# Kernel optimization log

Hardware: AMD Instinct MI355X
Metric: run time of the kernel (lower is better)

## Reference

```python
import jax, jax.numpy as jnp
import numpy as np

B, RES, C = 4, 128, 256
HW = RES * RES
H_FFT, W_FFT = RES, RES // 2 + 1
NUM_BANDS, GATE_HIDDEN = 6, 128
LN_EPS = 1e-5
FFT_NORM = 'ortho'
INIT_RANGE = 0.02


def _band_info(h_fft, w_fft, nb):
    # static radial band partition of the rFFT2 plane (matches RadialBandGate.__init__)
    yy = np.arange(h_fft, dtype=np.float32)[:, None] / max(h_fft - 1, 1)
    xx = np.arange(w_fft, dtype=np.float32)[None, :] / max(w_fft - 1, 1)
    r = np.sqrt(yy ** 2 + xx ** 2)
    r = r / (r.max() + 1e-8)
    bid = np.minimum(np.floor(r * nb), nb - 1).astype(np.int32).reshape(-1)  # (F,)
    onehot = np.zeros((bid.size, nb), dtype=np.float32)
    onehot[np.arange(bid.size), bid] = 1.0
    counts = np.maximum(onehot.sum(0), 1.0)
    return jnp.asarray(bid), jnp.asarray(onehot), jnp.asarray(counts)

BAND_ID, BAND_ONEHOT, BAND_COUNTS = _band_info(H_FFT, W_FFT, NUM_BANDS)


def setup_inputs() -> dict:
    key = jax.random.key(0)
    ks = jax.random.split(key, 16)
    return {
        'x': jax.random.normal(ks[0], (B, HW, C), jnp.float32),
        'time': jax.random.uniform(ks[1], (B,), jnp.float32),
        'w_real': jax.random.normal(ks[2], (C, C), jnp.float32) * INIT_RANGE,
        'w_imag': jax.random.normal(ks[3], (C, C), jnp.float32) * INIT_RANGE,
        'conv_w': jax.random.normal(ks[4], (C, 1, 3, 3), jnp.float32) * 0.1,  # depthwise
        'lin_w': jax.random.normal(ks[5], (C, C), jnp.float32) * 0.02,
        'lin_b': jnp.zeros((C,), jnp.float32),
        'mlp_w1': jax.random.normal(ks[6], (GATE_HIDDEN, NUM_BANDS), jnp.float32) * 0.3,
        'mlp_b1': jnp.zeros((GATE_HIDDEN,), jnp.float32),
        'mlp_w2': jax.random.normal(ks[7], (NUM_BANDS, GATE_HIDDEN), jnp.float32) * 0.1,
        'mlp_b2': jnp.zeros((NUM_BANDS,), jnp.float32),
        'norm_ww': jax.random.normal(ks[8], (C, 1), jnp.float32) * 0.02,  # ConditionalLayerNorm.weight Linear(1,dim)
        'norm_wb': jnp.ones((C,), jnp.float32),
        'norm_bw': jax.random.normal(ks[9], (C, 1), jnp.float32) * 0.02,
        'norm_bb': jnp.zeros((C,), jnp.float32),
        'kx': jnp.asarray(0.25, jnp.float32),
        'ky': jnp.asarray(0.25, jnp.float32),
    }


def _band_gate(feat, mlp_w1, mlp_b1, mlp_w2, mlp_b2):
    # feat: (B, C, F) real. scatter-add per band via one-hot matmul, mean, MLP, gather back.
    sums = jnp.einsum('bcf,fn->bcn', feat, BAND_ONEHOT)           # (B,C,NB)
    means = sums / (BAND_COUNTS + 1e-6)
    h = jax.nn.relu(jnp.einsum('bcn,hn->bch', means, mlp_w1) + mlp_b1)
    alpha_band = jax.nn.sigmoid(jnp.einsum('bch,nh->bcn', h, mlp_w2) + mlp_b2)
    return alpha_band[:, :, BAND_ID]                               # (B,C,F)


def reference(x, time, w_real, w_imag, conv_w, lin_w, lin_b,
              mlp_w1, mlp_b1, mlp_w2, mlp_b2,
              norm_ww, norm_wb, norm_bw, norm_bb, kx, ky):
    h = w = RES
    x2 = jnp.transpose(x.reshape(B, h, w, C), (0, 3, 1, 2))        # (B,C,h,w)
    Xf = jnp.fft.rfft2(x2, norm=FFT_NORM)                          # (B,C,h_fft,w_fft) complex

    # low-frequency rectangular mask (int(sigmoid(k)*dim) == floor for positive values)
    kx_i = jnp.floor(jax.nn.sigmoid(kx) * H_FFT)
    ky_i = jnp.floor(jax.nn.sigmoid(ky) * W_FFT)
    mask = ((jnp.arange(H_FFT)[:, None] < kx_i) & (jnp.arange(W_FFT)[None, :] < ky_i))
    Xf_low = Xf * mask[None, None].astype(Xf.real.dtype)

    F = H_FFT * W_FFT
    Xf_low_flat = Xf_low.reshape(B, C, F)
    W = w_real + 1j * w_imag                                       # (C,C) complex
    Xf_low_mapped = jnp.einsum('cd,bdf->bcf', W, Xf_low_flat).reshape(B, C, H_FFT, W_FFT)

    Xf_high = Xf - Xf_low
    feat_pred = jnp.abs(jnp.abs(Xf_high).reshape(B, C, F) - jnp.abs(Xf_low).reshape(B, C, F))
    alpha = _band_gate(feat_pred, mlp_w1, mlp_b1, mlp_w2, mlp_b2).reshape(B, C, H_FFT, W_FFT)

    Xf_fused = alpha * Xf_low_mapped + (1.0 - alpha) * Xf_high
    x_spec = jnp.fft.irfft2(Xf_fused, s=(h, w), norm=FFT_NORM)     # (B,C,h,w) real

    # depthwise 3x3 conv, padding=1, no bias
    xl = jax.lax.conv_general_dilated(x2, conv_w, window_strides=(1, 1), padding='SAME',
                                      feature_group_count=C,
                                      dimension_numbers=('NCHW', 'OIHW', 'NCHW'))
    # pointwise linear over channel dim
    xc = jnp.transpose((x @ lin_w.T + lin_b).reshape(B, h, w, C), (0, 3, 1, 2))

    y = jnp.transpose(x_spec + xl + xc, (0, 2, 3, 1)).reshape(B, HW, C)

    # ConditionalLayerNorm
    mean = y.mean(axis=-1, keepdims=True)
    var = (y ** 2).mean(axis=-1, keepdims=True) - mean ** 2
    yn = (y - mean) / jnp.sqrt(var + LN_EPS)
    t = time.reshape(-1, 1)                                        # (B,1)
    weight = (t @ norm_ww.T + norm_wb)[:, None, :]                 # (B,1,C)
    bias = (t @ norm_bw.T + norm_bb)[:, None, :]
    return weight * yn + bias
```

## Files before the change

kernel.cpp:

```cpp
#include <hip/hip_runtime.h>
#include <math.h>

#define B_ 4
#define C_ 256
#define RES_ 128
#define HW_ 16384
#define WF_ 65
#define F_ 8320
#define FP_ 2880

typedef __attribute__((ext_vector_type(8))) short bf16x8;
typedef __attribute__((ext_vector_type(16))) float f32x16;

__device__ __forceinline__ int brev7(int j){ return (int)(__brev((unsigned)j) >> 25); }
__device__ __forceinline__ int brev6(int j){ return (int)(__brev((unsigned)j) >> 26); }

__device__ __forceinline__ short f2bf(float f){
  unsigned u = __float_as_uint(f);
  unsigned r = (u + 0x7FFFu + ((u>>16)&1u)) >> 16;
  return (short)r;
}

__device__ __forceinline__ bf16x8 lds_frag(const short* p){
  union { bf16x8 v; int2 d[2]; } u;
  u.d[0] = *(const int2*)p;
  u.d[1] = *(const int2*)(p+4);
  return u.v;
}
__device__ __forceinline__ void lds_store8(short* p, bf16x8 v){
  union { bf16x8 v; int2 d[2]; } u; u.v = v;
  *(int2*)p = u.d[0]; *(int2*)(p+4) = u.d[1];
}

__device__ __forceinline__ int band_of(int row, int col){
  float yy = __fdiv_rn((float)row, 127.0f);
  float xx = __fdiv_rn((float)col, 64.0f);
  float rr = __fsqrt_rn(__fadd_rn(__fmul_rn(yy,yy), __fmul_rn(xx,xx)));
  float rm = __fadd_rn(__fsqrt_rn(2.0f), 1e-8f);
  float rn = __fdiv_rn(rr, rm);
  int b = (int)floorf(__fmul_rn(rn, 6.0f));
  return b > 5 ? 5 : b;
}

__device__ __forceinline__ float sigmoidf_(float v){ return 1.0f/(1.0f+expf(-v)); }

template<int SGN, int NROWS>
__device__ __forceinline__ void fft128_lds(float2* buf, int rstride, int tid, const float2* tw){
  const int total = NROWS*64;
  #pragma unroll
  for (int stage=0; stage<7; stage++){
    int half = 64 >> stage;
    __syncthreads();
    for (int idx = tid; idx < total; idx += 256){
      int row = idx % NROWS;
      int t   = idx / NROWS;
      int j   = t & (half-1);
      int i0  = ((t >> (6-stage)) << (7-stage)) + j;
      int i1  = i0 + half;
      float2* rb = buf + row*rstride;
      float2 a = rb[i0], b = rb[i1];
      float2 w = tw[j << stage];
      float dx = a.x - b.x, dy = a.y - b.y;
      rb[i0] = make_float2(a.x+b.x, a.y+b.y);
      float ws = (SGN < 0) ? -w.y : w.y;
      rb[i1] = make_float2(dx*w.x - dy*ws, dx*ws + dy*w.x);
    }
  }
  __syncthreads();
}

template<int SGN>
__device__ __forceinline__ float2 wave_fft64(float2 v, const float2* stw, int lane){
  #pragma unroll
  for (int s=0; s<6; s++){
    int H = 32 >> s;
    float ox = __shfl_xor(v.x, H);
    float oy = __shfl_xor(v.y, H);
    bool hi = (lane & H) != 0;
    float2 w = stw[s];
    float ws = (SGN < 0) ? -w.y : w.y;
    float sx = v.x + ox, sy = v.y + oy;
    float dx = ox - v.x, dy = oy - v.y;
    float rx = dx*w.x - dy*ws;
    float ry = dx*ws + dy*w.x;
    v.x = hi ? rx : sx;
    v.y = hi ? ry : sy;
  }
  return v;
}

__device__ __forceinline__ void make_stage_tw(float2* stw, int lane){
  #pragma unroll
  for (int s=0; s<6; s++){
    int H = 32 >> s;
    int t = (lane & (H-1)) << s;
    float sn, cs;
    sincosf(6.283185307179586f*(float)t/64.0f, &sn, &cs);
    stw[s] = make_float2(cs, sn);
  }
}

__global__ __launch_bounds__(1024) void k_transpose(const float* __restrict__ x, float* __restrict__ x2){
  __shared__ float tile[64][65];
  int b = blockIdx.z;
  int hw0 = blockIdx.x*64, c0 = blockIdx.y*64;
  int tx = threadIdx.x, ty = threadIdx.y;
  #pragma unroll
  for (int i=0;i<4;i++){
    int hw = hw0 + ty + i*16;
    tile[ty+i*16][tx] = x[((size_t)b*HW_ + hw)*C_ + c0 + tx];
  }
  __syncthreads();
  #pragma unroll
  for (int i=0;i<4;i++){
    int c = c0 + ty + i*16;
    x2[((size_t)b*C_ + c)*HW_ + hw0 + tx] = tile[tx][ty+i*16];
  }
}

__global__ __launch_bounds__(256) void k_counts(float* __restrict__ counts, unsigned char* __restrict__ bid){
  int tid = threadIdx.x;
  float acc[6] = {0,0,0,0,0,0};
  for (int f = tid; f < F_; f += 256){
    int row = f / WF_, col = f - row*WF_;
    int bnd = band_of(row, col);
    bid[f] = (unsigned char)bnd;
    #pragma unroll
    for (int n=0;n<6;n++) acc[n] += (bnd==n) ? 1.0f : 0.0f;
  }
  __shared__ float red[6][256];
  #pragma unroll
  for (int n=0;n<6;n++) red[n][tid] = acc[n];
  __syncthreads();
  for (int s=128; s>0; s>>=1){
    if (tid < s){
      #pragma unroll
      for (int n=0;n<6;n++) red[n][tid] += red[n][tid+s];
    }
    __syncthreads();
  }
  if (tid < 6) counts[tid] = fmaxf(red[tid][0], 1.0f);
}

__global__ __launch_bounds__(256) void k_wbf16(const float* __restrict__ wre, const float* __restrict__ wim,
                                               const float* __restrict__ lw,
                                               short* __restrict__ Wre, short* __restrict__ Wim,
                                               short* __restrict__ WL){
  int c = blockIdx.x, tid = threadIdx.x, plane = blockIdx.y;
  int idx = c*C_ + tid;
  if (plane == 0)      Wre[idx] = f2bf(wre[idx]);
  else if (plane == 1) Wim[idx] = f2bf(wim[idx]);
  else                 WL[idx]  = f2bf(lw[idx]);
}

__global__ __launch_bounds__(256) void k_fwd_rows(const float* __restrict__ x2, float2* __restrict__ X1){
  int tid = threadIdx.x;
  int lane = tid & 63, wv = tid >> 6;
  float2 stw[6];
  make_stage_tw(stw, lane);
  float sn128, cs128;
  sincosf(6.283185307179586f*(float)lane/128.0f, &sn128, &cs128);
  int slice = blockIdx.x >> 2;
  int r0 = (blockIdx.x & 3) * 32;
  const float* img = x2 + (size_t)slice*HW_ + (size_t)r0*128;
  float2* dst = X1 + (size_t)slice*F_ + (size_t)r0*WF_;
  #pragma unroll
  for (int i=0; i<8; i++){
    int row = wv*8 + i;
    float2 y = *(const float2*)(img + row*128 + lane*2);
    float2 v = wave_fft64<-1>(y, stw, lane);
    int rbk = brev6(lane);
    float2 Yk; Yk.x = __shfl(v.x, rbk); Yk.y = __shfl(v.y, rbk);
    int rbm = brev6((64 - lane) & 63);
    float2 Ym; Ym.x = __shfl(v.x, rbm); Ym.y = __shfl(v.y, rbm);
    float sx = Yk.x + Ym.x, sy = Yk.y - Ym.y;
    float dx = Yk.x - Ym.x, dy = Yk.y + Ym.y;
    dst[row*WF_ + lane] = make_float2(0.5f*(sx - sn128*dx + cs128*dy),
                                      0.5f*(sy - cs128*dx - sn128*dy));
    if (lane == 0)
      dst[row*WF_ + 64] = make_float2(Yk.x - Yk.y, 0.0f);
  }
}

__global__ __launch_bounds__(256) void k_fwd_cols_gate(const float2* __restrict__ X1, float2* __restrict__ Xf,
                                                       const float* __restrict__ counts, const unsigned char* __restrict__ bid,
                                                       const float* __restrict__ w1, const float* __restrict__ b1,
                                                       const float* __restrict__ w2, const float* __restrict__ b2,
                                                       float* __restrict__ alpha){
  __shared__ float2 cbuf[13*129];
  __shared__ float2 tw[64];
  __shared__ float red[6][256];
  __shared__ float means[6], h[128];
  int tid = threadIdx.x;
  if (tid < 64){ float s,c; sincosf(6.283185307179586f*(float)tid/128.0f,&s,&c); tw[tid]=make_float2(c,s); }
  int slice = blockIdx.x;
  const float2* xin = X1 + (size_t)slice*F_;
  float2* xout = Xf + (size_t)slice*F_;
  float acc[6] = {0,0,0,0,0,0};
  for (int chunk=0; chunk<5; chunk++){
    int c0 = chunk*13;
    __syncthreads();
    for (int p = tid; p < 13*128; p += 256){
      int y = p / 13, col = p - y*13;
      cbuf[col*129 + y] = xin[y*WF_ + c0 + col];
    }
    fft128_lds<-1,13>(cbuf, 129, tid, tw);
    for (int p = tid; p < 13*128; p += 256){
      int ky = p / 13, col = p - ky*13, kx = c0 + col;
      float2 v = cbuf[col*129 + brev7(ky)];
      v.x *= 0.0078125f; v.y *= 0.0078125f;
      int f = ky*WF_ + kx;
      xout[f] = v;
      float m = __fsqrt_rn(v.x*v.x + v.y*v.y);
      int bb = (int)bid[f];
      #pragma unroll
      for (int n=0;n<6;n++) acc[n] += (bb==n) ? m : 0.0f;
    }
  }
  __syncthreads();
  #pragma unroll
  for (int n=0;n<6;n++) red[n][tid] = acc[n];
  __syncthreads();
  for (int s=128; s>0; s>>=1){
    if (tid < s){
      #pragma unroll
      for (int n=0;n<6;n++) red[n][tid] += red[n][tid+s];
    }
    __syncthreads();
  }
  if (tid < 6) means[tid] = red[tid][0] / (counts[tid] + 1e-6f);
  __syncthreads();
  if (tid < 128){
    float hv = b1[tid];
    #pragma unroll
    for (int n=0;n<6;n++) hv += means[n]*w1[tid*6+n];
    h[tid] = fmaxf(hv, 0.0f);
  }
  __syncthreads();
  if (tid < 6){
    float o = b2[tid];
    for (int j=0;j<128;j++) o += h[j]*w2[tid*128+j];
    alpha[slice*6 + tid] = sigmoidf_(o);
  }
}

__global__ __launch_bounds__(256) void k_xt(const float2* __restrict__ Xf,
                                            short* __restrict__ XtRe, short* __restrict__ XtIm){
  __shared__ float2 tile[40][129];
  int tid = threadIdx.x;
  int ky = blockIdx.x, d0 = blockIdx.y*128, b = blockIdx.z;
  const float2* xb = Xf + ((size_t)(b*C_ + d0))*F_ + ky*WF_;
  #pragma unroll
  for (int i=0;i<20;i++){
    int p = tid + i*256;
    int d = p / 40, kx = p - d*40;
    tile[kx][d] = xb[(size_t)d*F_ + kx];
  }
  __syncthreads();
  #pragma unroll
  for (int i=0;i<20;i++){
    int p = tid + i*256;
    int kx = p >> 7, d = p & 127;
    float2 v = tile[kx][d];
    size_t o = ((size_t)b*FP_ + ky*40 + kx)*C_ + d0 + d;
    XtRe[o] = f2bf(v.x);
    XtIm[o] = f2bf(v.y);
  }
}

__global__ __launch_bounds__(256) void k_mix_mfma(const short* __restrict__ Wre, const short* __restrict__ Wim,
                                                  const short* __restrict__ XtRe, const short* __restrict__ XtIm,
                                                  const float* __restrict__ kxp, const float* __restrict__ kyp,
                                                  float2* __restrict__ mappedP){
  __shared__ short Are[64][36], Aim[64][36], Bre[64][36], Bim[64][36];
  int tid = threadIdx.x;
  int fp0 = blockIdx.x*64, c0 = blockIdx.y*64, b = blockIdx.z;
  int lane = tid & 63, w = tid >> 6;
  int mt = (w >> 1)*32, nt = (w & 1)*32;
  f32x16 accre = {0.f,0.f,0.f,0.f,0.f,0.f,0.f,0.f,0.f,0.f,0.f,0.f,0.f,0.f,0.f,0.f};
  f32x16 accim = {0.f,0.f,0.f,0.f,0.f,0.f,0.f,0.f,0.f,0.f,0.f,0.f,0.f,0.f,0.f,0.f};
  const short* xrb = XtRe + ((size_t)b*FP_ + fp0)*C_;
  const short* xib = XtIm + ((size_t)b*FP_ + fp0)*C_;
  int row4 = tid >> 2, part = tid & 3;
  for (int kc=0; kc<8; kc++){
    int d0 = kc*32;
    __syncthreads();
    lds_store8(&Are[row4][part*8], *(const bf16x8*)&Wre[(c0+row4)*C_ + d0 + part*8]);
    lds_store8(&Aim[row4][part*8], *(const bf16x8*)&Wim[(c0+row4)*C_ + d0 + part*8]);
    lds_store8(&Bre[row4][part*8], *(const bf16x8*)&xrb[(size_t)row4*C_ + d0 + part*8]);
    lds_store8(&Bim[row4][part*8], *(const bf16x8*)&xib[(size_t)row4*C_ + d0 + part*8]);
    __syncthreads();
    #pragma unroll
    for (int ks=0; ks<2; ks++){
      int koff = ks*16 + (lane>>5)*8;
      bf16x8 are = lds_frag(&Are[mt + (lane&31)][koff]);
      bf16x8 aim = lds_frag(&Aim[mt + (lane&31)][koff]);
      bf16x8 bre = lds_frag(&Bre[nt + (lane&31)][koff]);
      bf16x8 bim = lds_frag(&Bim[nt + (lane&31)][koff]);
      bf16x8 naim;
      { union { bf16x8 v; unsigned u[4]; } t1, t2; t1.v = aim;
        #pragma unroll
        for (int j=0;j<4;j++) t2.u[j] = t1.u[j] ^ 0x80008000u;
        naim = t2.v; }
      accre = __builtin_amdgcn_mfma_f32_32x32x16_bf16(are,  bre, accre, 0,0,0);
      accre = __builtin_amdgcn_mfma_f32_32x32x16_bf16(naim, bim, accre, 0,0,0);
      accim = __builtin_amdgcn_mfma_f32_32x32x16_bf16(are,  bim, accim, 0,0,0);
      accim = __builtin_amdgcn_mfma_f32_32x32x16_bf16(aim,  bre, accim, 0,0,0);
    }
  }
  float rowlim = floorf(sigmoidf_(kxp[0])*128.0f);
  float collim = floorf(sigmoidf_(kyp[0])*65.0f);
  int n = fp0 + nt + (lane & 31);
  int ky = n / 40, kx = n - ky*40;
  bool live = ((float)ky < rowlim) && ((float)kx < collim);
  #pragma unroll
  for (int reg=0; reg<16; reg++){
    int r = (reg & 3) + 8*(reg >> 2) + 4*(lane >> 5);
    int c = c0 + mt + r;
    if (live)
      mappedP[((size_t)(b*C_ + c))*FP_ + n] = make_float2(accre[reg], accim[reg]);
  }
}

__global__ __launch_bounds__(256) void k_pw_mfma(const float* __restrict__ x, const short* __restrict__ WL,
                                                  const float* __restrict__ lb, float* __restrict__ xcs){
  __shared__ short As[64][36], Bs[64][36];
  int tid = threadIdx.x;
  int hw0 = blockIdx.x*64, c0 = blockIdx.y*64, b = blockIdx.z;
  int lane = tid & 63, w = tid >> 6;
  int mt = (w >> 1)*32, nt = (w & 1)*32;
  f32x16 acc = {0.f,0.f,0.f,0.f,0.f,0.f,0.f,0.f,0.f,0.f,0.f,0.f,0.f,0.f,0.f,0.f};
  const float* xb = x + ((size_t)b*HW_ + hw0)*C_;
  int row4 = tid >> 2, part = tid & 3;
  for (int kc=0; kc<8; kc++){
    int d0 = kc*32;
    __syncthreads();
    lds_store8(&As[row4][part*8], *(const bf16x8*)&WL[(c0+row4)*C_ + d0 + part*8]);
    {
      const float* src = &xb[(size_t)row4*C_ + d0 + part*8];
      float4 va = *(const float4*)src;
      float4 vb = *(const float4*)(src+4);
      bf16x8 bv;
      bv[0]=f2bf(va.x); bv[1]=f2bf(va.y); bv[2]=f2bf(va.z); bv[3]=f2bf(va.w);
      bv[4]=f2bf(vb.x); bv[5]=f2bf(vb.y); bv[6]=f2bf(vb.z); bv[7]=f2bf(vb.w);
      lds_store8(&Bs[row4][part*8], bv);
    }
    __syncthreads();
    #pragma unroll
    for (int ks=0; ks<2; ks++){
      int koff = ks*16 + (lane>>5)*8;
      bf16x8 a  = lds_frag(&As[mt + (lane&31)][koff]);
      bf16x8 bb = lds_frag(&Bs[nt + (lane&31)][koff]);
      acc = __builtin_amdgcn_mfma_f32_32x32x16_bf16(a, bb, acc, 0,0,0);
    }
  }
  int n = hw0 + nt + (lane & 31);
  #pragma unroll
  for (int reg=0; reg<16; reg++){
    int r = (reg & 3) + 8*(reg >> 2) + 4*(lane >> 5);
    int c = c0 + mt + r;
    xcs[((size_t)(b*C_ + c))*HW_ + n] = acc[reg] + lb[c];
  }
}

__global__ __launch_bounds__(256) void k_inv_cols(float2* __restrict__ XfY, const float2* __restrict__ mappedP,
                                                  const float* __restrict__ alpha, const unsigned char* __restrict__ bid,
                                                  const float* __restrict__ kxp, const float* __restrict__ kyp){
  __shared__ float2 cbuf[13*129];
  __shared__ float2 tw[64];
  __shared__ float al[6];
  int tid = threadIdx.x;
  int chunk = blockIdx.x, slice = blockIdx.y;
  int c0 = chunk*13;
  if (tid < 64){ float s,c; sincosf(6.283185307179586f*(float)tid/128.0f,&s,&c); tw[tid]=make_float2(c,s); }
  if (tid < 6) al[tid] = alpha[slice*6 + tid];
  float rowlim = floorf(sigmoidf_(kxp[0])*128.0f);
  float collim = floorf(sigmoidf_(kyp[0])*65.0f);
  __syncthreads();
  float2* xfb = XfY + (size_t)slice*F_;
  const float2* mpb = mappedP + (size_t)slice*FP_;
  for (int p = tid; p < 13*128; p += 256){
    int ky = p / 13, col = p - ky*13, kx = c0 + col;
    int f = ky*WF_ + kx;
    float a = al[(int)bid[f]];
    bool inm = ((float)ky < rowlim) && ((float)kx < collim);
    float2 v;
    if (inm){ v = mpb[ky*40 + kx]; v.x *= a; v.y *= a; }
    else    { v = xfb[f]; float om = 1.0f - a; v.x *= om; v.y *= om; }
    cbuf[col*129 + ky] = v;
  }
  fft128_lds<1,13>(cbuf, 129, tid, tw);
  for (int p = tid; p < 13*128; p += 256){
    int y = p / 13, col = p - y*13;
    xfb[y*WF_ + c0 + col] = cbuf[col*129 + brev7(y)];
  }
}

__global__ __launch_bounds__(256) void k_inv_rows(const float2* __restrict__ Y1, const float* __restrict__ xcs,
                                                  const float* __restrict__ x2, const float* __restrict__ cw,
                                                  float* __restrict__ sbuf){
  __shared__ float ct[34*128];
  int tid = threadIdx.x;
  int lane = tid & 63, wv = tid >> 6;
  float2 stw[6];
  make_stage_tw(stw, lane);
  float sn128, cs128;
  sincosf(6.283185307179586f*(float)lane/128.0f, &sn128, &cs128);
  int slice = blockIdx.x >> 2;
  int ch = slice & 255;
  int r0 = (blockIdx.x & 3) * 32;
  const float* img = x2 + (size_t)slice*HW_;
  #pragma unroll
  for (int q=0;q<17;q++){
    int p = tid + q*256;
    int row = p >> 7, xx = p & 127;
    int sr = r0 - 1 + row;
    ct[p] = ((unsigned)sr < 128u) ? img[sr*128+xx] : 0.0f;
  }
  float w9[9];
  #pragma unroll
  for (int k=0;k<9;k++) w9[k] = cw[ch*9+k];
  __syncthreads();
  const float2* src = Y1 + (size_t)slice*F_ + (size_t)r0*WF_;
  size_t gbase = (size_t)slice*HW_ + (size_t)r0*128;
  #pragma unroll
  for (int i=0;i<8;i++){
    int row = wv*8 + i;
    const float2* rs = src + row*WF_;
    float2 a = rs[lane];
    float2 b = rs[64 - lane];
    if (lane == 0){ a.y = 0.0f; b.y = 0.0f; }
    float sx = a.x + b.x, sy = a.y - b.y;
    float dx = a.x - b.x, dy = a.y + b.y;
    float2 yk = make_float2(0.5f*(sx - sn128*dx - cs128*dy),
                            0.5f*(sy + cs128*dx - sn128*dy));
    float2 v = wave_fft64<1>(yk, stw, lane);
    int rbk = brev6(lane);
    float2 z; z.x = __shfl(v.x, rbk); z.y = __shfl(v.y, rbk);
    int xx = lane << 1;
    float c0 = 0.0f, c1 = 0.0f;
    #pragma unroll
    for (int dy2=0; dy2<3; dy2++){
      const float* cr = &ct[(row+dy2)*128];
      float l  = (xx>0)    ? cr[xx-1] : 0.0f;
      float mm = cr[xx];
      float r  = cr[xx+1];
      float rr = (xx<126)  ? cr[xx+2] : 0.0f;
      c0 += l*w9[dy2*3+0] + mm*w9[dy2*3+1] + r*w9[dy2*3+2];
      c1 += mm*w9[dy2*3+0] + r*w9[dy2*3+1] + rr*w9[dy2*3+2];
    }
    size_t g = gbase + (size_t)(row*128 + xx);
    float2 xc = *(const float2*)&xcs[g];
    float2 o;
    o.x = z.x*0.015625f + xc.x + c0;
    o.y = z.y*0.015625f + xc.y + c1;
    *(float2*)&sbuf[g] = o;
  }
}

__global__ __launch_bounds__(256) void k_stats(const float* __restrict__ sbuf, float* __restrict__ stats){
  int g = blockIdx.x*256 + threadIdx.x;
  int b = g >> 14, hw = g & 16383;
  const float* p = sbuf + (size_t)b*C_*HW_ + hw;
  float s1 = 0.0f, s2 = 0.0f;
  for (int c=0; c<C_; c++){
    float v = p[(size_t)c*HW_];
    s1 += v; s2 += v*v;
  }
  float mean = s1 * (1.0f/256.0f);
  float var  = s2 * (1.0f/256.0f) - mean*mean;
  stats[g] = mean;
  stats[65536 + g] = 1.0f / sqrtf(var + 1e-5f);
}

__global__ __launch_bounds__(256) void k_apply(const float* __restrict__ sbuf, const float* __restrict__ stats,
                                               const float* __restrict__ timev,
                                               const float* __restrict__ nww, const float* __restrict__ nwb,
                                               const float* __restrict__ nbw, const float* __restrict__ nbb,
                                               float* __restrict__ out){
  __shared__ float tile[64][65];
  __shared__ float wv[64], bv[64], mv[64], rv[64];
  int b = blockIdx.z, c0 = blockIdx.y*64, hw0 = blockIdx.x*64;
  int tid = threadIdx.x;
  if (tid < 64){
    float t = timev[b];
    int c = c0 + tid;
    wv[tid] = t*nww[c] + nwb[c];
    bv[tid] = t*nbw[c] + nbb[c];
    mv[tid] = stats[(b<<14) + hw0 + tid];
    rv[tid] = stats[65536 + (b<<14) + hw0 + tid];
  }
  #pragma unroll
  for (int q=0;q<16;q++){
    int p = tid + q*256;
    int cl = p >> 6, hwl = p & 63;
    tile[cl][hwl] = sbuf[((size_t)(b*C_+c0+cl))*HW_ + hw0 + hwl];
  }
  __syncthreads();
  #pragma unroll
  for (int q=0;q<16;q++){
    int p = tid + q*256;
    int hwl = p >> 6, cl = p & 63;
    float v = tile[cl][hwl];
    out[((size_t)(b*HW_+hw0+hwl))*C_ + c0 + cl] = wv[cl]*((v - mv[hwl])*rv[hwl]) + bv[cl];
  }
}

extern "C" void kernel_launch(void* const* d_in, const int* in_sizes, int n_in,
                              void* d_out, int out_size, void* d_ws, size_t ws_size,
                              hipStream_t stream){
  const float* x      = (const float*)d_in[0];
  const float* timev  = (const float*)d_in[1];
  const float* w_real = (const float*)d_in[2];
  const float* w_imag = (const float*)d_in[3];
  const float* conv_w = (const float*)d_in[4];
  const float* lin_w  = (const float*)d_in[5];
  const float* lin_b  = (const float*)d_in[6];
  const float* mlp_w1 = (const float*)d_in[7];
  const float* mlp_b1 = (const float*)d_in[8];
  const float* mlp_w2 = (const float*)d_in[9];
  const float* mlp_b2 = (const float*)d_in[10];
  const float* norm_ww= (const float*)d_in[11];
  const float* norm_wb= (const float*)d_in[12];
  const float* norm_bw= (const float*)d_in[13];
  const float* norm_bb= (const float*)d_in[14];
  const float* kxp    = (const float*)d_in[15];
  const float* kyp    = (const float*)d_in[16];

  float* ws = (float*)d_ws;
  float*  alpha  = ws;
  unsigned char* bid = (unsigned char*)(ws + 6144);
  float*  counts = ws + 8224;
  float*  stats  = ws + 8288;
  short*  Wre_bf = (short*)(ws + 139360);
  short*  Wim_bf = (short*)(ws + 172128);
  short*  WL_bf  = (short*)(ws + 204896);
  float*  x2     = ws + 237664;
  float2* Xf     = (float2*)(ws + 17014880);
  float*  CbF    = ws + 34054240;
  float2* X1     = (float2*)CbF;
  short*  XtRe   = (short*)CbF;
  short*  XtIm   = (short*)(CbF + 1474560);
  float2* mappedP= (float2*)(CbF + 2949120);
  float*  sb     = CbF;
  float*  xcs    = (float*)d_out;
  float*  out    = (float*)d_out;

  k_transpose    <<<dim3(256, 4, B_), dim3(64,16), 0, stream>>>(x, x2);
  k_counts       <<<1, 256, 0, stream>>>(counts, bid);
  k_wbf16        <<<dim3(256, 3), 256, 0, stream>>>(w_real, w_imag, lin_w, Wre_bf, Wim_bf, WL_bf);
  k_fwd_rows     <<<4096, 256, 0, stream>>>(x2, X1);
  k_fwd_cols_gate<<<1024, 256, 0, stream>>>(X1, Xf, counts, bid, mlp_w1, mlp_b1, mlp_w2, mlp_b2, alpha);
  k_xt           <<<dim3(72, 2, B_), 256, 0, stream>>>(Xf, XtRe, XtIm);
  k_pw_mfma      <<<dim3(256, 4, B_), 256, 0, stream>>>(x, WL_bf, lin_b, xcs);
  k_mix_mfma     <<<dim3(45, 4, B_), 256, 0, stream>>>(Wre_bf, Wim_bf, XtRe, XtIm, kxp, kyp, mappedP);
  k_inv_cols     <<<dim3(5, 1024), 256, 0, stream>>>(Xf, mappedP, alpha, bid, kxp, kyp);
  k_inv_rows     <<<4096, 256, 0, stream>>>((const float2*)Xf, xcs, x2, conv_w, sb);
  k_stats        <<<256, 256, 0, stream>>>(sb, stats);
  k_apply        <<<dim3(256, 4, B_), 256, 0, stream>>>(sb, stats, timev, norm_ww, norm_wb, norm_bw, norm_bb, out);
}
```

Measured before the change: 483.5 us.

## Store spectrum column-major and do column FFTs with wave-level shuffles

Changes the intermediate spectrum layout from row-major (ky, kx) to kx-major so each 128-point column FFT reads contiguous memory. The LDS-based radix-2 column FFT with 7 barrier stages is replaced by a split into two 64-point wave-shuffle FFTs per wave. Row FFT kernels now transpose through shared memory tiles on write and read, and the band-id table, the mixing-kernel index mapping and the k_xt gather are updated to the new layout. This is meant to remove the barrier-heavy LDS FFT and strided column accesses, at the cost of extra LDS transposes in the row kernels.

New measurement: 450.7 us. -6.8%, faster.

```diff
diff --git a/kernel.cpp b/kernel.cpp
--- a/kernel.cpp
+++ b/kernel.cpp
@@ -12,7 +12,6 @@
 typedef __attribute__((ext_vector_type(8))) short bf16x8;
 typedef __attribute__((ext_vector_type(16))) float f32x16;
 
-__device__ __forceinline__ int brev7(int j){ return (int)(__brev((unsigned)j) >> 25); }
 __device__ __forceinline__ int brev6(int j){ return (int)(__brev((unsigned)j) >> 26); }
 
 __device__ __forceinline__ short f2bf(float f){
@@ -43,31 +42,6 @@
 }
 
 __device__ __forceinline__ float sigmoidf_(float v){ return 1.0f/(1.0f+expf(-v)); }
-
-template<int SGN, int NROWS>
-__device__ __forceinline__ void fft128_lds(float2* buf, int rstride, int tid, const float2* tw){
-  const int total = NROWS*64;
-  #pragma unroll
-  for (int stage=0; stage<7; stage++){
-    int half = 64 >> stage;
-    __syncthreads();
-    for (int idx = tid; idx < total; idx += 256){
-      int row = idx % NROWS;
-      int t   = idx / NROWS;
-      int j   = t & (half-1);
-      int i0  = ((t >> (6-stage)) << (7-stage)) + j;
-      int i1  = i0 + half;
-      float2* rb = buf + row*rstride;
-      float2 a = rb[i0], b = rb[i1];
-      float2 w = tw[j << stage];
-      float dx = a.x - b.x, dy = a.y - b.y;
-      rb[i0] = make_float2(a.x+b.x, a.y+b.y);
-      float ws = (SGN < 0) ? -w.y : w.y;
-      rb[i1] = make_float2(dx*w.x - dy*ws, dx*ws + dy*w.x);
-    }
-  }
-  __syncthreads();
-}
 
 template<int SGN>
 __device__ __forceinline__ float2 wave_fft64(float2 v, const float2* stw, int lane){
@@ -100,6 +74,17 @@
   }
 }
 
+__device__ __forceinline__ void redist2(float2 a0, float2 a1, int lane, float2& u0, float2& u1){
+  int s0 = lane >> 1, s1 = s0 + 32;
+  bool odd = (lane & 1) != 0;
+  float t0x = __shfl(a0.x, s0), t0y = __shfl(a0.y, s0);
+  float t1x = __shfl(a1.x, s0), t1y = __shfl(a1.y, s0);
+  u0 = odd ? make_float2(t1x, t1y) : make_float2(t0x, t0y);
+  float q0x = __shfl(a0.x, s1), q0y = __shfl(a0.y, s1);
+  float q1x = __shfl(a1.x, s1), q1y = __shfl(a1.y, s1);
+  u1 = odd ? make_float2(q1x, q1y) : make_float2(q0x, q0y);
+}
+
 __global__ __launch_bounds__(1024) void k_transpose(const float* __restrict__ x, float* __restrict__ x2){
   __shared__ float tile[64][65];
   int b = blockIdx.z;
@@ -118,13 +103,13 @@
   }
 }
 
-__global__ __launch_bounds__(256) void k_counts(float* __restrict__ counts, unsigned char* __restrict__ bid){
+__global__ __launch_bounds__(256) void k_counts(float* __restrict__ counts, unsigned char* __restrict__ bid_t){
   int tid = threadIdx.x;
   float acc[6] = {0,0,0,0,0,0};
-  for (int f = tid; f < F_; f += 256){
-    int row = f / WF_, col = f - row*WF_;
-    int bnd = band_of(row, col);
-    bid[f] = (unsigned char)bnd;
+  for (int p = tid; p < F_; p += 256){
+    int kx = p >> 7, ky = p & 127;
+    int bnd = band_of(ky, kx);
+    bid_t[p] = (unsigned char)bnd;
     #pragma unroll
     for (int n=0;n<6;n++) acc[n] += (bnd==n) ? 1.0f : 0.0f;
   }
@@ -153,7 +138,8 @@
   else                 WL[idx]  = f2bf(lw[idx]);
 }
 
-__global__ __launch_bounds__(256) void k_fwd_rows(const float* __restrict__ x2, float2* __restrict__ X1){
+__global__ __launch_bounds__(256) void k_fwd_rows(const float* __restrict__ x2, float2* __restrict__ X1t){
+  __shared__ float2 tile[65*33];
   int tid = threadIdx.x;
   int lane = tid & 63, wv = tid >> 6;
   float2 stw[6];
@@ -163,11 +149,10 @@
   int slice = blockIdx.x >> 2;
   int r0 = (blockIdx.x & 3) * 32;
   const float* img = x2 + (size_t)slice*HW_ + (size_t)r0*128;
-  float2* dst = X1 + (size_t)slice*F_ + (size_t)r0*WF_;
   #pragma unroll
   for (int i=0; i<8; i++){
-    int row = wv*8 + i;
-    float2 y = *(const float2*)(img + row*128 + lane*2);
+    int rr = wv*8 + i;
+    float2 y = *(const float2*)(img + rr*128 + lane*2);
     float2 v = wave_fft64<-1>(y, stw, lane);
     int rbk = brev6(lane);
     float2 Yk; Yk.x = __shfl(v.x, rbk); Yk.y = __shfl(v.y, rbk);
@@ -175,49 +160,60 @@
     float2 Ym; Ym.x = __shfl(v.x, rbm); Ym.y = __shfl(v.y, rbm);
     float sx = Yk.x + Ym.x, sy = Yk.y - Ym.y;
     float dx = Yk.x - Ym.x, dy = Yk.y + Ym.y;
-    dst[row*WF_ + lane] = make_float2(0.5f*(sx - sn128*dx + cs128*dy),
-                                      0.5f*(sy - cs128*dx - sn128*dy));
+    tile[lane*33 + rr] = make_float2(0.5f*(sx - sn128*dx + cs128*dy),
+                                     0.5f*(sy - cs128*dx - sn128*dy));
     if (lane == 0)
-      dst[row*WF_ + 64] = make_float2(Yk.x - Yk.y, 0.0f);
-  }
-}
-
-__global__ __launch_bounds__(256) void k_fwd_cols_gate(const float2* __restrict__ X1, float2* __restrict__ Xf,
-                                                       const float* __restrict__ counts, const unsigned char* __restrict__ bid,
+      tile[64*33 + rr] = make_float2(Yk.x - Yk.y, 0.0f);
+  }
+  __syncthreads();
+  float2* dst = X1t + (size_t)slice*F_ + r0;
+  for (int p = tid; p < 65*32; p += 256){
+    int kx = p >> 5, rr = p & 31;
+    dst[(size_t)kx*128 + rr] = tile[kx*33 + rr];
+  }
+}
+
+__global__ __launch_bounds__(256) void k_fwd_cols_gate(const float2* __restrict__ X1t, float2* __restrict__ Xft,
+                                                       const float* __restrict__ counts, const unsigned char* __restrict__ bid_t,
                                                        const float* __restrict__ w1, const float* __restrict__ b1,
                                                        const float* __restrict__ w2, const float* __restrict__ b2,
                                                        float* __restrict__ alpha){
-  __shared__ float2 cbuf[13*129];
-  __shared__ float2 tw[64];
   __shared__ float red[6][256];
   __shared__ float means[6], h[128];
   int tid = threadIdx.x;
-  if (tid < 64){ float s,c; sincosf(6.283185307179586f*(float)tid/128.0f,&s,&c); tw[tid]=make_float2(c,s); }
+  int lane = tid & 63, wv = tid >> 6;
+  float2 stw[6];
+  make_stage_tw(stw, lane);
+  float sn128, cs128;
+  sincosf(6.283185307179586f*(float)lane/128.0f, &sn128, &cs128);
   int slice = blockIdx.x;
-  const float2* xin = X1 + (size_t)slice*F_;
-  float2* xout = Xf + (size_t)slice*F_;
+  const float2* xin = X1t + (size_t)slice*F_;
+  float2* xout = Xft + (size_t)slice*F_;
   float acc[6] = {0,0,0,0,0,0};
-  for (int chunk=0; chunk<5; chunk++){
-    int c0 = chunk*13;
-    __syncthreads();
-    for (int p = tid; p < 13*128; p += 256){
-      int y = p / 13, col = p - y*13;
-      cbuf[col*129 + y] = xin[y*WF_ + c0 + col];
-    }
-    fft128_lds<-1,13>(cbuf, 129, tid, tw);
-    for (int p = tid; p < 13*128; p += 256){
-      int ky = p / 13, col = p - ky*13, kx = c0 + col;
-      float2 v = cbuf[col*129 + brev7(ky)];
-      v.x *= 0.0078125f; v.y *= 0.0078125f;
-      int f = ky*WF_ + kx;
-      xout[f] = v;
-      float m = __fsqrt_rn(v.x*v.x + v.y*v.y);
-      int bb = (int)bid[f];
-      #pragma unroll
-      for (int n=0;n<6;n++) acc[n] += (bb==n) ? m : 0.0f;
-    }
-  }
-  __syncthreads();
+  for (int kx = wv; kx < 65; kx += 4){
+    float4 rv = *(const float4*)(xin + (size_t)kx*128 + (lane<<1));
+    float2 a0 = make_float2(rv.x, rv.y), a1 = make_float2(rv.z, rv.w);
+    float2 u0, u1;
+    redist2(a0, a1, lane, u0, u1);
+    float2 s = make_float2(u0.x+u1.x, u0.y+u1.y);
+    float ddx = u0.x-u1.x, ddy = u0.y-u1.y;
+    float2 dw = make_float2(ddx*cs128 + ddy*sn128, ddy*cs128 - ddx*sn128);
+    float2 v0 = wave_fft64<-1>(s, stw, lane);
+    float2 v1 = wave_fft64<-1>(dw, stw, lane);
+    int rb = brev6(lane);
+    float ex = __shfl(v0.x, rb), ey = __shfl(v0.y, rb);
+    float ox = __shfl(v1.x, rb), oy = __shfl(v1.y, rb);
+    ex *= 0.0078125f; ey *= 0.0078125f;
+    ox *= 0.0078125f; oy *= 0.0078125f;
+    float4 wvout = make_float4(ex, ey, ox, oy);
+    *(float4*)(xout + (size_t)kx*128 + (lane<<1)) = wvout;
+    float me = __fsqrt_rn(ex*ex + ey*ey);
+    float mo = __fsqrt_rn(ox*ox + oy*oy);
+    int be = (int)bid_t[kx*128 + (lane<<1)];
+    int bo = (int)bid_t[kx*128 + (lane<<1) + 1];
+    #pragma unroll
+    for (int n=0;n<6;n++) acc[n] += ((be==n) ? me : 0.0f) + ((bo==n) ? mo : 0.0f);
+  }
   #pragma unroll
   for (int n=0;n<6;n++) red[n][tid] = acc[n];
   __syncthreads();
@@ -244,27 +240,26 @@
   }
 }
 
-__global__ __launch_bounds__(256) void k_xt(const float2* __restrict__ Xf,
+__global__ __launch_bounds__(256) void k_xt(const float2* __restrict__ Xft,
                                             short* __restrict__ XtRe, short* __restrict__ XtIm){
-  __shared__ float2 tile[40][129];
-  int tid = threadIdx.x;
-  int ky = blockIdx.x, d0 = blockIdx.y*128, b = blockIdx.z;
-  const float2* xb = Xf + ((size_t)(b*C_ + d0))*F_ + ky*WF_;
-  #pragma unroll
-  for (int i=0;i<20;i++){
-    int p = tid + i*256;
-    int d = p / 40, kx = p - d*40;
-    tile[kx][d] = xb[(size_t)d*F_ + kx];
-  }
-  __syncthreads();
-  #pragma unroll
-  for (int i=0;i<20;i++){
-    int p = tid + i*256;
-    int kx = p >> 7, d = p & 127;
-    float2 v = tile[kx][d];
-    size_t o = ((size_t)b*FP_ + ky*40 + kx)*C_ + d0 + d;
-    XtRe[o] = f2bf(v.x);
-    XtIm[o] = f2bf(v.y);
+  __shared__ short sre[72*130];
+  __shared__ short sim[72*130];
+  int tid = threadIdx.x;
+  int kx = blockIdx.x, d0 = blockIdx.y*128, b = blockIdx.z;
+  const float2* xb = Xft + ((size_t)(b*C_ + d0))*F_ + (size_t)kx*128;
+  for (int p = tid; p < 72*128; p += 256){
+    int d = p / 72, ky = p - d*72;
+    float2 v = xb[(size_t)d*F_ + ky];
+    sre[ky*130 + d] = f2bf(v.x);
+    sim[ky*130 + d] = f2bf(v.y);
+  }
+  __syncthreads();
+  short* dre = XtRe + ((size_t)b*FP_ + (size_t)kx*72)*C_ + d0;
+  short* dim_ = XtIm + ((size_t)b*FP_ + (size_t)kx*72)*C_ + d0;
+  for (int p = tid; p < 72*128; p += 256){
+    int ky = p >> 7, d = p & 127;
+    dre[(size_t)ky*C_ + d] = sre[ky*130 + d];
+    dim_[(size_t)ky*C_ + d] = sim[ky*130 + d];
   }
 }
 
@@ -311,7 +306,7 @@
   float rowlim = floorf(sigmoidf_(kxp[0])*128.0f);
   float collim = floorf(sigmoidf_(kyp[0])*65.0f);
   int n = fp0 + nt + (lane & 31);
-  int ky = n / 40, kx = n - ky*40;
+  int ky = n % 72, kx = n / 72;
   bool live = ((float)ky < rowlim) && ((float)kx < collim);
   #pragma unroll
   for (int reg=0; reg<16; reg++){
@@ -363,43 +358,61 @@
   }
 }
 
-__global__ __launch_bounds__(256) void k_inv_cols(float2* __restrict__ XfY, const float2* __restrict__ mappedP,
-                                                  const float* __restrict__ alpha, const unsigned char* __restrict__ bid,
+__global__ __launch_bounds__(256) void k_inv_cols(float2* __restrict__ XftY, const float2* __restrict__ mappedP,
+                                                  const float* __restrict__ alpha, const unsigned char* __restrict__ bid_t,
                                                   const float* __restrict__ kxp, const float* __restrict__ kyp){
-  __shared__ float2 cbuf[13*129];
-  __shared__ float2 tw[64];
   __shared__ float al[6];
   int tid = threadIdx.x;
-  int chunk = blockIdx.x, slice = blockIdx.y;
-  int c0 = chunk*13;
-  if (tid < 64){ float s,c; sincosf(6.283185307179586f*(float)tid/128.0f,&s,&c); tw[tid]=make_float2(c,s); }
+  int lane = tid & 63, wv = tid >> 6;
+  int slice = blockIdx.x;
+  float2 stw[6];
+  make_stage_tw(stw, lane);
+  float sn128, cs128;
+  sincosf(6.283185307179586f*(float)lane/128.0f, &sn128, &cs128);
   if (tid < 6) al[tid] = alpha[slice*6 + tid];
   float rowlim = floorf(sigmoidf_(kxp[0])*128.0f);
   float collim = floorf(sigmoidf_(kyp[0])*65.0f);
   __syncthreads();
-  float2* xfb = XfY + (size_t)slice*F_;
+  float2* xfb = XftY + (size_t)slice*F_;
   const float2* mpb = mappedP + (size_t)slice*FP_;
-  for (int p = tid; p < 13*128; p += 256){
-    int ky = p / 13, col = p - ky*13, kx = c0 + col;
-    int f = ky*WF_ + kx;
-    float a = al[(int)bid[f]];
-    bool inm = ((float)ky < rowlim) && ((float)kx < collim);
-    float2 v;
-    if (inm){ v = mpb[ky*40 + kx]; v.x *= a; v.y *= a; }
-    else    { v = xfb[f]; float om = 1.0f - a; v.x *= om; v.y *= om; }
-    cbuf[col*129 + ky] = v;
-  }
-  fft128_lds<1,13>(cbuf, 129, tid, tw);
-  for (int p = tid; p < 13*128; p += 256){
-    int y = p / 13, col = p - y*13;
-    xfb[y*WF_ + c0 + col] = cbuf[col*129 + brev7(y)];
-  }
-}
-
-__global__ __launch_bounds__(256) void k_inv_rows(const float2* __restrict__ Y1, const float* __restrict__ xcs,
+  for (int kx = wv; kx < 65; kx += 4){
+    float4 rv = *(const float4*)(xfb + (size_t)kx*128 + (lane<<1));
+    int ky0 = lane << 1;
+    float a_e = al[(int)bid_t[kx*128 + ky0]];
+    float a_o = al[(int)bid_t[kx*128 + ky0 + 1]];
+    bool cok  = ((float)kx < collim);
+    bool in_e = cok && ((float)ky0 < rowlim);
+    bool in_o = cok && ((float)(ky0+1) < rowlim);
+    float2 ve, vo;
+    if (in_e){
+      float4 mv = *(const float4*)(mpb + (size_t)kx*72 + ky0);
+      ve = make_float2(mv.x*a_e, mv.y*a_e);
+      vo = in_o ? make_float2(mv.z*a_o, mv.w*a_o)
+                : make_float2(rv.z*(1.0f-a_o), rv.w*(1.0f-a_o));
+    } else {
+      ve = make_float2(rv.x*(1.0f-a_e), rv.y*(1.0f-a_e));
+      vo = make_float2(rv.z*(1.0f-a_o), rv.w*(1.0f-a_o));
+    }
+    float2 u0, u1;
+    redist2(ve, vo, lane, u0, u1);
+    float2 s = make_float2(u0.x+u1.x, u0.y+u1.y);
+    float ddx = u0.x-u1.x, ddy = u0.y-u1.y;
+    float2 dw = make_float2(ddx*cs128 - ddy*sn128, ddx*sn128 + ddy*cs128);
+    float2 v0 = wave_fft64<1>(s, stw, lane);
+    float2 v1 = wave_fft64<1>(dw, stw, lane);
+    int rb = brev6(lane);
+    float4 outv;
+    outv.x = __shfl(v0.x, rb); outv.y = __shfl(v0.y, rb);
+    outv.z = __shfl(v1.x, rb); outv.w = __shfl(v1.y, rb);
+    *(float4*)(xfb + (size_t)kx*128 + (lane<<1)) = outv;
+  }
+}
+
+__global__ __launch_bounds__(256) void k_inv_rows(const float2* __restrict__ Y1t, const float* __restrict__ xcs,
                                                   const float* __restrict__ x2, const float* __restrict__ cw,
                                                   float* __restrict__ sbuf){
   __shared__ float ct[34*128];
+  __shared__ float2 ytile[65*33];
   int tid = threadIdx.x;
   int lane = tid & 63, wv = tid >> 6;
   float2 stw[6];
@@ -417,18 +430,21 @@
     int sr = r0 - 1 + row;
     ct[p] = ((unsigned)sr < 128u) ? img[sr*128+xx] : 0.0f;
   }
+  const float2* ysrc = Y1t + (size_t)slice*F_ + r0;
+  for (int p = tid; p < 65*32; p += 256){
+    int kx = p >> 5, rr = p & 31;
+    ytile[kx*33 + rr] = ysrc[(size_t)kx*128 + rr];
+  }
   float w9[9];
   #pragma unroll
   for (int k=0;k<9;k++) w9[k] = cw[ch*9+k];
   __syncthreads();
-  const float2* src = Y1 + (size_t)slice*F_ + (size_t)r0*WF_;
   size_t gbase = (size_t)slice*HW_ + (size_t)r0*128;
   #pragma unroll
   for (int i=0;i<8;i++){
     int row = wv*8 + i;
-    const float2* rs = src + row*WF_;
-    float2 a = rs[lane];
-    float2 b = rs[64 - lane];
+    float2 a = ytile[lane*33 + row];
+    float2 b = ytile[(64-lane)*33 + row];
     if (lane == 0){ a.y = 0.0f; b.y = 0.0f; }
     float sx = a.x + b.x, sy = a.y - b.y;
     float dx = a.x - b.x, dy = a.y + b.y;
@@ -529,16 +545,16 @@
 
   float* ws = (float*)d_ws;
   float*  alpha  = ws;
-  unsigned char* bid = (unsigned char*)(ws + 6144);
+  unsigned char* bid_t = (unsigned char*)(ws + 6144);
   float*  counts = ws + 8224;
   float*  stats  = ws + 8288;
   short*  Wre_bf = (short*)(ws + 139360);
   short*  Wim_bf = (short*)(ws + 172128);
   short*  WL_bf  = (short*)(ws + 204896);
   float*  x2     = ws + 237664;
-  float2* Xf     = (float2*)(ws + 17014880);
+  float2* Xft    = (float2*)(ws + 17014880);
   float*  CbF    = ws + 34054240;
-  float2* X1     = (float2*)CbF;
+  float2* X1t    = (float2*)CbF;
   short*  XtRe   = (short*)CbF;
   short*  XtIm   = (short*)(CbF + 1474560);
   float2* mappedP= (float2*)(CbF + 2949120);
@@ -547,15 +563,15 @@
   float*  out    = (float*)d_out;
 
   k_transpose    <<<dim3(256, 4, B_), dim3(64,16), 0, stream>>>(x, x2);
-  k_counts       <<<1, 256, 0, stream>>>(counts, bid);
+  k_counts       <<<1, 256, 0, stream>>>(counts, bid_t);
   k_wbf16        <<<dim3(256, 3), 256, 0, stream>>>(w_real, w_imag, lin_w, Wre_bf, Wim_bf, WL_bf);
-  k_fwd_rows     <<<4096, 256, 0, stream>>>(x2, X1);
-  k_fwd_cols_gate<<<1024, 256, 0, stream>>>(X1, Xf, counts, bid, mlp_w1, mlp_b1, mlp_w2, mlp_b2, alpha);
-  k_xt           <<<dim3(72, 2, B_), 256, 0, stream>>>(Xf, XtRe, XtIm);
+  k_fwd_rows     <<<4096, 256, 0, stream>>>(x2, X1t);
+  k_fwd_cols_gate<<<1024, 256, 0, stream>>>(X1t, Xft, counts, bid_t, mlp_w1, mlp_b1, mlp_w2, mlp_b2, alpha);
+  k_xt           <<<dim3(40, 2, B_), 256, 0, stream>>>(Xft, XtRe, XtIm);
   k_pw_mfma      <<<dim3(256, 4, B_), 256, 0, stream>>>(x, WL_bf, lin_b, xcs);
   k_mix_mfma     <<<dim3(45, 4, B_), 256, 0, stream>>>(Wre_bf, Wim_bf, XtRe, XtIm, kxp, kyp, mappedP);
-  k_inv_cols     <<<dim3(5, 1024), 256, 0, stream>>>(Xf, mappedP, alpha, bid, kxp, kyp);
-  k_inv_rows     <<<4096, 256, 0, stream>>>((const float2*)Xf, xcs, x2, conv_w, sb);
+  k_inv_cols     <<<1024, 256, 0, stream>>>(Xft, mappedP, alpha, bid_t, kxp, kyp);
+  k_inv_rows     <<<4096, 256, 0, stream>>>((const float2*)Xft, xcs, x2, conv_w, sb);
   k_stats        <<<256, 256, 0, stream>>>(sb, stats);
   k_apply        <<<dim3(256, 4, B_), 256, 0, stream>>>(sb, stats, timev, norm_ww, norm_wb, norm_bw, norm_bb, out);
 }
```
